# Optimization experiments

Measured on AMD Instinct MI355X. Metric: run time of the kernel, lower is better.

The kernel has to match this reference:

```python
import jax, jax.numpy as jnp
import numpy as np

D_MODEL = 1024
NHEAD = 16
HEAD_DIM = D_MODEL // NHEAD
NEG = -1e9
LN_EPS = 1e-5


def setup_inputs() -> dict:
    key = jax.random.key(0)
    ks = jax.random.split(key, 12)
    B, S, D = 2, 2048, D_MODEL
    scale = 1.0 / np.sqrt(D)
    inp = {
        "x": jax.random.normal(ks[0], (B, S, D), jnp.float32),
        "mask": jax.random.randint(ks[1], (B, S), 0, 2, jnp.int32),
        "wq": jax.random.normal(ks[2], (D, D), jnp.float32) * scale,
        "bq": jnp.zeros((D,), jnp.float32),
        "wk": jax.random.normal(ks[3], (D, D), jnp.float32) * scale,
        "bk": jnp.zeros((D,), jnp.float32),
        "wv": jax.random.normal(ks[4], (D, D), jnp.float32) * scale,
        "bv": jnp.zeros((D,), jnp.float32),
        "wo": jax.random.normal(ks[5], (D, D), jnp.float32) * scale,
        "bo": jnp.zeros((D,), jnp.float32),
        "attn_bias": jax.random.normal(ks[6], (1, NHEAD, 1, 1), jnp.float32) * 0.02,
        "ln_g": jnp.ones((D,), jnp.float32),
        "ln_b": jnp.zeros((D,), jnp.float32),
    }
    return inp


def _layer_norm(x, g, b):
    mu = jnp.mean(x, axis=-1, keepdims=True)
    var = jnp.var(x, axis=-1, keepdims=True)
    return (x - mu) * jax.lax.rsqrt(var + LN_EPS) * g + b


def reference(x, mask, wq, bq, wk, bk, wv, bv, wo, bo, attn_bias, ln_g, ln_b):
    B, S, D = x.shape
    H, Hd = NHEAD, HEAD_DIM
    # QKV projections -> [B, H, S, Hd]
    q = (x @ wq + bq).reshape(B, S, H, Hd).transpose(0, 2, 1, 3)
    k = (x @ wk + bk).reshape(B, S, H, Hd).transpose(0, 2, 1, 3)
    v = (x @ wv + bv).reshape(B, S, H, Hd).transpose(0, 2, 1, 3)
    # Scores [B, H, S, S] with per-head scalar bias
    scores = jnp.einsum("bhsd,bhtd->bhst", q, k) / jnp.sqrt(jnp.float32(Hd))
    scores = scores + attn_bias
    # mask [B,S] -> [B,1,1,S]; masked_fill where mask == 0
    m = (mask[:, None, None, :] == 0)
    scores = jnp.where(m, jnp.float32(NEG), scores)
    attn = jax.nn.softmax(scores, axis=-1)  # dropout = identity (eval)
    out = jnp.einsum("bhst,bhtd->bhsd", attn, v)
    out = out.transpose(0, 2, 1, 3).reshape(B, S, D)
    out = out @ wo + bo
    return _layer_norm(x + out, ln_g, ln_b)
```

## Files before the change

kernel.cpp:

```cpp
#include <hip/hip_runtime.h>

typedef __attribute__((ext_vector_type(8))) short short8;
typedef __attribute__((ext_vector_type(4))) float f32x4;
typedef __attribute__((ext_vector_type(16))) float f32x16;
typedef __attribute__((ext_vector_type(4))) unsigned short us4;

#define DEV __device__ __forceinline__

#define GLD16(gp, lp) __builtin_amdgcn_global_load_lds( \
    (const __attribute__((address_space(1))) void*)(gp), \
    (__attribute__((address_space(3))) void*)(lp), 16, 0, 0)

DEV unsigned short f2bf(float f) {
    union { float f; unsigned u; } v; v.f = f;
    unsigned r = v.u + 0x7fffu + ((v.u >> 16) & 1u);
    return (unsigned short)(r >> 16);
}

DEV float fexp2(float x) {
#if __has_builtin(__builtin_amdgcn_exp2f)
    return __builtin_amdgcn_exp2f(x);
#else
    return __expf(x * 0.69314718056f);
#endif
}

__global__ __launch_bounds__(256) void k_convert(const float* __restrict__ x,
                                                 unsigned short* __restrict__ xb) {
    int i = blockIdx.x * 256 + threadIdx.x;
    float4 v = ((const float4*)x)[i];
    us4 o = { f2bf(v.x), f2bf(v.y), f2bf(v.z), f2bf(v.w) };
    ((us4*)xb)[i] = o;
}

__global__ __launch_bounds__(256) void k_transw(const float* __restrict__ wq, const float* __restrict__ wk,
                                                const float* __restrict__ wv, const float* __restrict__ wo,
                                                unsigned short* __restrict__ wt) {
    __shared__ float tile[32][33];
    const int z = blockIdx.z;
    const float* src = (z == 0) ? wq : (z == 1) ? wk : (z == 2) ? wv : wo;
    unsigned short* dst = wt + (size_t)z * (1u << 20);
    const int n0 = blockIdx.x * 32, k0 = blockIdx.y * 32;
    const int tx = threadIdx.x, ty = threadIdx.y;
#pragma unroll
    for (int i = 0; i < 4; ++i)
        tile[ty + i * 8][tx] = src[(size_t)(k0 + ty + i * 8) * 1024 + n0 + tx];
    __syncthreads();
#pragma unroll
    for (int i = 0; i < 4; ++i)
        dst[(size_t)(n0 + ty + i * 8) * 1024 + k0 + tx] = f2bf(tile[tx][ty + i * 8]);
}

template <int MODE>
__global__ __launch_bounds__(256) void k_gemm(const unsigned short* __restrict__ A,
                                              const unsigned short* __restrict__ Wt,
                                              const float* __restrict__ bias,
                                              void* __restrict__ out, float scale) {
    __shared__ unsigned short lA[2][128 * 32];
    __shared__ unsigned short lB[2][64 * 32];
    const int m0 = blockIdx.y * 128, n0 = blockIdx.x * 64;
    const int tid = threadIdx.x;
    const int lane = tid & 63;
    const int w = tid >> 6, wm = w >> 1, wn = w & 1;

    const int arow0 = tid >> 2, acl = tid & 3;
    const int arow1 = (tid + 256) >> 2;
    const int brow = tid >> 2;
    const unsigned short* agp0 = A + (size_t)(m0 + arow0) * 1024 + acl * 8;
    const unsigned short* agp1 = A + (size_t)(m0 + arow1) * 1024 + acl * 8;
    const unsigned short* bgp  = Wt + (size_t)(n0 + brow) * 1024 + acl * 8;
    const int apc0 = ((arow0 << 2) | (acl ^ ((arow0 >> 1) & 3))) * 8;
    const int apc1 = ((arow1 << 2) | (acl ^ ((arow1 >> 1) & 3))) * 8;
    const int bpc  = ((brow  << 2) | (acl ^ ((brow  >> 1) & 3))) * 8;

    int ach[4], bch[2];
#pragma unroll
    for (int mt = 0; mt < 4; ++mt) {
        int row = wm * 64 + mt * 16 + (lane & 15);
        ach[mt] = ((row << 2) | ((lane >> 4) ^ ((row >> 1) & 3))) * 8;
    }
#pragma unroll
    for (int nt = 0; nt < 2; ++nt) {
        int row = wn * 32 + nt * 16 + (lane & 15);
        bch[nt] = ((row << 2) | ((lane >> 4) ^ ((row >> 1) & 3))) * 8;
    }

    f32x4 acc[4][2] = {};
    short8 ra0 = *(const short8*)agp0;
    short8 ra1 = *(const short8*)agp1;
    short8 rb0 = *(const short8*)bgp;

    for (int t = 0; t < 32; ++t) {
        unsigned short* sA = lA[t & 1];
        unsigned short* sB = lB[t & 1];
        *(short8*)(sA + apc0) = ra0;
        *(short8*)(sA + apc1) = ra1;
        *(short8*)(sB + bpc)  = rb0;
        if (t < 31) {
            ra0 = *(const short8*)(agp0 + (t + 1) * 32);
            ra1 = *(const short8*)(agp1 + (t + 1) * 32);
            rb0 = *(const short8*)(bgp  + (t + 1) * 32);
        }
        __syncthreads();
        short8 af[4], bf[2];
#pragma unroll
        for (int mt = 0; mt < 4; ++mt) af[mt] = *(const short8*)(sA + ach[mt]);
#pragma unroll
        for (int nt = 0; nt < 2; ++nt) bf[nt] = *(const short8*)(sB + bch[nt]);
#pragma unroll
        for (int mt = 0; mt < 4; ++mt)
#pragma unroll
            for (int nt = 0; nt < 2; ++nt)
                acc[mt][nt] = __builtin_amdgcn_mfma_f32_16x16x32_bf16(af[mt], bf[nt], acc[mt][nt], 0, 0, 0);
    }

#pragma unroll
    for (int nt = 0; nt < 2; ++nt) {
        const int col = n0 + wn * 32 + nt * 16 + (lane & 15);
        const float bv = bias[col];
#pragma unroll
        for (int mt = 0; mt < 4; ++mt) {
#pragma unroll
            for (int r = 0; r < 4; ++r) {
                const int row = m0 + wm * 64 + mt * 16 + (lane >> 4) * 4 + r;
                const float v = (acc[mt][nt][r] + bv) * scale;
                if (MODE == 0) {
                    int b = row >> 11, s = row & 2047, h = col >> 6, hd = col & 63;
                    ((unsigned short*)out)[(size_t)((b * 16 + h) * 2048 + s) * 64 + hd] = f2bf(v);
                } else if (MODE == 1) {
                    int b = row >> 11, s = row & 2047, h = col >> 6, hd = col & 63;
                    ((unsigned short*)out)[(size_t)((b * 16 + h) * 64 + hd) * 2048 + s] = f2bf(v);
                } else {
                    ((float*)out)[(size_t)row * 1024 + col] = v;
                }
            }
        }
    }
}

__global__ __launch_bounds__(256, 2) void k_attn(const unsigned short* __restrict__ Qb,
                                                 const unsigned short* __restrict__ Kb,
                                                 const unsigned short* __restrict__ Vt,
                                                 const int* __restrict__ mask,
                                                 const float* __restrict__ attn_bias,
                                                 unsigned short* __restrict__ ao) {
    __shared__ unsigned short ksm[2 * 4096];
    __shared__ unsigned short vsm[2 * 4096];
    __shared__ float addb[2048];
    __shared__ float lbuf[128];
    const int id = blockIdx.x;
    const int xcd = id & 7, slot = id >> 3;
    const int bh = xcd * 4 + (slot >> 4), qt = slot & 15;
    const int b = bh >> 4, h = bh & 15;
    const int tid = threadIdx.x, l = tid & 63, w = tid >> 6;
    const int q = l & 31, hi = l >> 5;

    {
        const float hb = attn_bias[h] * 1.44269504f;
        const int4* m4 = (const int4*)(mask + b * 2048);
#pragma unroll
        for (int i = 0; i < 2; ++i) {
            int idx = tid + i * 256;
            int4 m = m4[idx];
            float4 a = { m.x ? hb : -1e30f, m.y ? hb : -1e30f,
                         m.z ? hb : -1e30f, m.w ? hb : -1e30f };
            ((float4*)addb)[idx] = a;
        }
    }

    const size_t bhS = (size_t)bh * 2048;
    const unsigned short* Kbh = Kb + bhS * 64;
    const unsigned short* Vbh = Vt + (size_t)bh * 64 * 2048;
    const int q0 = qt * 128 + w * 32;

    const int srow = l >> 3;
    const int sxor = 8 * ((l & 7) ^ ((l >> 3) & 7));
    const unsigned short* Ksrc = Kbh + (size_t)(w * 16 + srow) * 64 + sxor;
    const unsigned short* Vsrc = Vbh + (size_t)(w * 16 + srow) * 2048 + sxor;
    unsigned short* lk0 = ksm + w * 1024;
    unsigned short* lv0 = vsm + w * 1024;

#define STAGE(kt_, buf_) { \
    const unsigned short* gk = Ksrc + (size_t)(kt_) * 4096; \
    const unsigned short* gv = Vsrc + (kt_) * 64; \
    unsigned short* lk = lk0 + (buf_) * 4096; \
    unsigned short* lv = lv0 + (buf_) * 4096; \
    GLD16(gk, lk); GLD16(gk + 512, lk + 512); \
    GLD16(gv, lv); GLD16(gv + 16384, lv + 512); }

    int kro[2][4], vro[2][2][2];
#pragma unroll
    for (int sub = 0; sub < 2; ++sub) {
#pragma unroll
        for (int db = 0; db < 4; ++db) {
            int key = q + sub * 32;
            kro[sub][db] = key * 128 + ((db * 32 + hi * 16) ^ ((key & 7) << 4));
        }
#pragma unroll
        for (int kg = 0; kg < 2; ++kg)
#pragma unroll
            for (int dh = 0; dh < 2; ++dh) {
                int row = q + dh * 32;
                vro[sub][kg][dh] = row * 128 + ((sub * 64 + kg * 32 + hi * 16) ^ ((row & 7) << 4));
            }
    }

    short8 qf[4];
#pragma unroll
    for (int db = 0; db < 4; ++db)
        qf[db] = *(const short8*)(Qb + (bhS + q0 + q) * 64 + db * 16 + hi * 8);

    f32x16 o0 = {}, o1 = {};
    float4 ls = { 0.f, 0.f, 0.f, 0.f };

    STAGE(0, 0);
    __syncthreads();

    for (int kt = 0; kt < 32; ++kt) {
        const int cur = kt & 1;
        if (kt < 31) STAGE(kt + 1, cur ^ 1);
        const char* kb = (const char*)(ksm + cur * 4096);
        const char* vb = (const char*)(vsm + cur * 4096);
        const float* abp = addb + kt * 64;
#pragma unroll
        for (int sub = 0; sub < 2; ++sub) {
            short8 kf0 = *(const short8*)(kb + kro[sub][0]);
            short8 kf1 = *(const short8*)(kb + kro[sub][1]);
            short8 kf2 = *(const short8*)(kb + kro[sub][2]);
            short8 kf3 = *(const short8*)(kb + kro[sub][3]);
            f32x16 sa0 = {}, sa1 = {};
            __builtin_amdgcn_s_setprio(1);
            sa0 = __builtin_amdgcn_mfma_f32_32x32x16_bf16(kf0, qf[0], sa0, 0, 0, 0);
            sa1 = __builtin_amdgcn_mfma_f32_32x32x16_bf16(kf1, qf[1], sa1, 0, 0, 0);
            sa0 = __builtin_amdgcn_mfma_f32_32x32x16_bf16(kf2, qf[2], sa0, 0, 0, 0);
            sa1 = __builtin_amdgcn_mfma_f32_32x32x16_bf16(kf3, qf[3], sa1, 0, 0, 0);
            __builtin_amdgcn_s_setprio(0);
            float p[16];
#pragma unroll
            for (int rr = 0; rr < 4; ++rr) {
                float4 ab = *(const float4*)(abp + sub * 32 + rr * 8 + hi * 4);
                p[rr * 4 + 0] = fexp2(sa0[rr * 4 + 0] + sa1[rr * 4 + 0] + ab.x);
                p[rr * 4 + 1] = fexp2(sa0[rr * 4 + 1] + sa1[rr * 4 + 1] + ab.y);
                p[rr * 4 + 2] = fexp2(sa0[rr * 4 + 2] + sa1[rr * 4 + 2] + ab.z);
                p[rr * 4 + 3] = fexp2(sa0[rr * 4 + 3] + sa1[rr * 4 + 3] + ab.w);
            }
#pragma unroll
            for (int r = 0; r < 16; r += 4) {
                ls.x += p[r]; ls.y += p[r + 1]; ls.z += p[r + 2]; ls.w += p[r + 3];
            }
#pragma unroll
            for (int kg = 0; kg < 2; ++kg) {
                unsigned P0, P1, P2, P3;
                asm("v_cvt_pk_bf16_f32 %0, %1, %2" : "=v"(P0) : "v"(p[kg * 8 + 0]), "v"(p[kg * 8 + 1]));
                asm("v_cvt_pk_bf16_f32 %0, %1, %2" : "=v"(P1) : "v"(p[kg * 8 + 2]), "v"(p[kg * 8 + 3]));
                asm("v_cvt_pk_bf16_f32 %0, %1, %2" : "=v"(P2) : "v"(p[kg * 8 + 4]), "v"(p[kg * 8 + 5]));
                asm("v_cvt_pk_bf16_f32 %0, %1, %2" : "=v"(P3) : "v"(p[kg * 8 + 6]), "v"(p[kg * 8 + 7]));
                asm("v_permlane32_swap_b32 %0, %1" : "+v"(P0), "+v"(P2));
                asm("v_permlane32_swap_b32 %0, %1" : "+v"(P1), "+v"(P3));
                union { unsigned u[4]; short8 s8; } af;
                af.u[0] = P0; af.u[1] = P1; af.u[2] = P2; af.u[3] = P3;
                short8 vf0 = *(const short8*)(vb + vro[sub][kg][0]);
                short8 vf1 = *(const short8*)(vb + vro[sub][kg][1]);
                __builtin_amdgcn_s_setprio(1);
                o0 = __builtin_amdgcn_mfma_f32_32x32x16_bf16(af.s8, vf0, o0, 0, 0, 0);
                o1 = __builtin_amdgcn_mfma_f32_32x32x16_bf16(af.s8, vf1, o1, 0, 0, 0);
                __builtin_amdgcn_s_setprio(0);
            }
        }
        __syncthreads();
    }

    float lsum = ls.x + ls.y + ls.z + ls.w;
    lsum += __shfl_xor(lsum, 32, 64);
    if (hi == 0) lbuf[w * 32 + q] = lsum;
    __syncthreads();
    float4 linv[4];
#pragma unroll
    for (int rr = 0; rr < 4; ++rr) {
        float4 lv = *(const float4*)(lbuf + w * 32 + rr * 8 + hi * 4);
        linv[rr] = { __builtin_amdgcn_rcpf(lv.x), __builtin_amdgcn_rcpf(lv.y),
                     __builtin_amdgcn_rcpf(lv.z), __builtin_amdgcn_rcpf(lv.w) };
    }
    unsigned short* aop = ao + ((size_t)b * 2048 + q0) * 1024 + h * 64 + q;
#pragma unroll
    for (int r = 0; r < 16; ++r) {
        int qrow = (r & 3) + 8 * (r >> 2) + 4 * hi;
        aop[(size_t)qrow * 1024] = f2bf(o0[r] * linv[r >> 2][r & 3]);
        aop[(size_t)qrow * 1024 + 32] = f2bf(o1[r] * linv[r >> 2][r & 3]);
    }
#undef STAGE
}

__global__ __launch_bounds__(256) void k_ln(const float* __restrict__ x, const float* __restrict__ op,
                                            const float* __restrict__ g, const float* __restrict__ be,
                                            float* __restrict__ out) {
    const int row = blockIdx.x, tid = threadIdx.x;
    const float4 xv = ((const float4*)(x + (size_t)row * 1024))[tid];
    const float4 ov = ((const float4*)(op + (size_t)row * 1024))[tid];
    float4 v = { xv.x + ov.x, xv.y + ov.y, xv.z + ov.z, xv.w + ov.w };
    float sum = v.x + v.y + v.z + v.w;
    float ss = v.x * v.x + v.y * v.y + v.z * v.z + v.w * v.w;
#pragma unroll
    for (int xm = 1; xm < 64; xm <<= 1) {
        sum += __shfl_xor(sum, xm, 64);
        ss += __shfl_xor(ss, xm, 64);
    }
    __shared__ float red[8];
    const int lane = tid & 63, w = tid >> 6;
    if (lane == 0) { red[w] = sum; red[4 + w] = ss; }
    __syncthreads();
    sum = red[0] + red[1] + red[2] + red[3];
    ss = red[4] + red[5] + red[6] + red[7];
    const float mu = sum * (1.0f / 1024.0f);
    const float rstd = rsqrtf(ss * (1.0f / 1024.0f) - mu * mu + 1e-5f);
    const float4 gv = ((const float4*)g)[tid];
    const float4 bv = ((const float4*)be)[tid];
    float4 o = { (v.x - mu) * rstd * gv.x + bv.x, (v.y - mu) * rstd * gv.y + bv.y,
                 (v.z - mu) * rstd * gv.z + bv.z, (v.w - mu) * rstd * gv.w + bv.w };
    ((float4*)(out + (size_t)row * 1024))[tid] = o;
}

extern "C" void kernel_launch(void* const* d_in, const int* in_sizes, int n_in,
                              void* d_out, int out_size, void* d_ws, size_t ws_size,
                              hipStream_t stream) {
    const float* x        = (const float*)d_in[0];
    const int*   mask     = (const int*)d_in[1];
    const float* wq       = (const float*)d_in[2];
    const float* bq       = (const float*)d_in[3];
    const float* wk       = (const float*)d_in[4];
    const float* bk       = (const float*)d_in[5];
    const float* wv       = (const float*)d_in[6];
    const float* bv       = (const float*)d_in[7];
    const float* wo       = (const float*)d_in[8];
    const float* bo       = (const float*)d_in[9];
    const float* attnb    = (const float*)d_in[10];
    const float* ln_g     = (const float*)d_in[11];
    const float* ln_b     = (const float*)d_in[12];

    char* ws = (char*)d_ws;
    unsigned short* xb  = (unsigned short*)(ws);
    unsigned short* wt  = (unsigned short*)(ws + (8ll  << 20));
    unsigned short* qb  = (unsigned short*)(ws + (16ll << 20));
    unsigned short* kb  = (unsigned short*)(ws + (24ll << 20));
    unsigned short* vtb = (unsigned short*)(ws + (32ll << 20));
    unsigned short* ao  = (unsigned short*)(ws + (40ll << 20));
    float*          opj = (float*)(ws + (48ll << 20));

    const float qscale = 0.125f * 1.44269504f;

    k_convert<<<4096, 256, 0, stream>>>(x, xb);
    k_transw<<<dim3(32, 32, 4), dim3(32, 8), 0, stream>>>(wq, wk, wv, wo, wt);
    k_gemm<0><<<dim3(16, 32), 256, 0, stream>>>(xb, wt,              bq, (void*)qb, qscale);
    k_gemm<0><<<dim3(16, 32), 256, 0, stream>>>(xb, wt + (1u << 20), bk, (void*)kb, 1.0f);
    k_gemm<1><<<dim3(16, 32), 256, 0, stream>>>(xb, wt + (2u << 20), bv, (void*)vtb, 1.0f);
    k_attn<<<512, 256, 0, stream>>>(qb, kb, vtb, mask, attnb, ao);
    k_gemm<2><<<dim3(16, 32), 256, 0, stream>>>(ao, wt + (3u << 20), bo, (void*)opj, 1.0f);
    k_ln<<<4096, 256, 0, stream>>>(x, opj, ln_g, ln_b, (float*)d_out);
}
```

Before: 148.5 us.

## Split attention over key halves, async-load GEMM tiles, bf16 output projection

Attention now splits each query tile across two key halves, giving 1024 blocks at higher occupancy. Each half writes unnormalized partial outputs and row sums, and a new combine kernel adds them and normalizes. The GEMM swaps register-staged tile loads for direct global-to-LDS loads with double buffering. The output projection is written as bf16 instead of fp32 to reduce traffic into layernorm, at the cost of an extra kernel launch, an extra round trip for the partials and lower precision in the residual add.

```diff
diff --git a/kernel.cpp b/kernel.cpp
--- a/kernel.cpp
+++ b/kernel.cpp
@@ -15,6 +15,11 @@
     union { float f; unsigned u; } v; v.f = f;
     unsigned r = v.u + 0x7fffu + ((v.u >> 16) & 1u);
     return (unsigned short)(r >> 16);
+}
+
+DEV float bf2f(unsigned short u) {
+    union { unsigned u; float f; } v; v.u = (unsigned)u << 16;
+    return v.f;
 }
 
 DEV float fexp2(float x) {
@@ -63,15 +68,18 @@
     const int lane = tid & 63;
     const int w = tid >> 6, wm = w >> 1, wn = w & 1;
 
-    const int arow0 = tid >> 2, acl = tid & 3;
-    const int arow1 = (tid + 256) >> 2;
-    const int brow = tid >> 2;
-    const unsigned short* agp0 = A + (size_t)(m0 + arow0) * 1024 + acl * 8;
-    const unsigned short* agp1 = A + (size_t)(m0 + arow1) * 1024 + acl * 8;
-    const unsigned short* bgp  = Wt + (size_t)(n0 + brow) * 1024 + acl * 8;
-    const int apc0 = ((arow0 << 2) | (acl ^ ((arow0 >> 1) & 3))) * 8;
-    const int apc1 = ((arow1 << 2) | (acl ^ ((arow1 >> 1) & 3))) * 8;
-    const int bpc  = ((brow  << 2) | (acl ^ ((brow  >> 1) & 3))) * 8;
+    const int srow = tid >> 2;
+    const int scl = (tid & 3) ^ ((tid >> 3) & 3);
+    const unsigned short* aSrc0 = A + (size_t)(m0 + srow) * 1024 + scl * 8;
+    const unsigned short* aSrc1 = A + (size_t)(m0 + 64 + srow) * 1024 + scl * 8;
+    const unsigned short* bSrc  = Wt + (size_t)(n0 + srow) * 1024 + scl * 8;
+
+#define GSTAGE(t_, buf_) { \
+    unsigned short* sA_ = lA[buf_] + w * 512; \
+    unsigned short* sB_ = lB[buf_] + w * 512; \
+    GLD16(aSrc0 + (t_) * 32, sA_); \
+    GLD16(aSrc1 + (t_) * 32, sA_ + 2048); \
+    GLD16(bSrc  + (t_) * 32, sB_); }
 
     int ach[4], bch[2];
 #pragma unroll
@@ -86,22 +94,14 @@
     }
 
     f32x4 acc[4][2] = {};
-    short8 ra0 = *(const short8*)agp0;
-    short8 ra1 = *(const short8*)agp1;
-    short8 rb0 = *(const short8*)bgp;
+    GSTAGE(0, 0);
+    __syncthreads();
 
     for (int t = 0; t < 32; ++t) {
-        unsigned short* sA = lA[t & 1];
-        unsigned short* sB = lB[t & 1];
-        *(short8*)(sA + apc0) = ra0;
-        *(short8*)(sA + apc1) = ra1;
-        *(short8*)(sB + bpc)  = rb0;
-        if (t < 31) {
-            ra0 = *(const short8*)(agp0 + (t + 1) * 32);
-            ra1 = *(const short8*)(agp1 + (t + 1) * 32);
-            rb0 = *(const short8*)(bgp  + (t + 1) * 32);
-        }
-        __syncthreads();
+        const int cur = t & 1;
+        if (t < 31) GSTAGE(t + 1, cur ^ 1);
+        const unsigned short* sA = lA[cur];
+        const unsigned short* sB = lB[cur];
         short8 af[4], bf[2];
 #pragma unroll
         for (int mt = 0; mt < 4; ++mt) af[mt] = *(const short8*)(sA + ach[mt]);
@@ -112,7 +112,9 @@
 #pragma unroll
             for (int nt = 0; nt < 2; ++nt)
                 acc[mt][nt] = __builtin_amdgcn_mfma_f32_16x16x32_bf16(af[mt], bf[nt], acc[mt][nt], 0, 0, 0);
-    }
+        __syncthreads();
+    }
+#undef GSTAGE
 
 #pragma unroll
     for (int nt = 0; nt < 2; ++nt) {
@@ -131,52 +133,49 @@
                     int b = row >> 11, s = row & 2047, h = col >> 6, hd = col & 63;
                     ((unsigned short*)out)[(size_t)((b * 16 + h) * 64 + hd) * 2048 + s] = f2bf(v);
                 } else {
-                    ((float*)out)[(size_t)row * 1024 + col] = v;
+                    ((unsigned short*)out)[(size_t)row * 1024 + col] = f2bf(v);
                 }
             }
         }
     }
 }
 
-__global__ __launch_bounds__(256, 2) void k_attn(const unsigned short* __restrict__ Qb,
+__global__ __launch_bounds__(256, 4) void k_attn(const unsigned short* __restrict__ Qb,
                                                  const unsigned short* __restrict__ Kb,
                                                  const unsigned short* __restrict__ Vt,
                                                  const int* __restrict__ mask,
                                                  const float* __restrict__ attn_bias,
-                                                 unsigned short* __restrict__ ao) {
+                                                 unsigned short* __restrict__ po0,
+                                                 unsigned short* __restrict__ po1,
+                                                 float* __restrict__ lp0,
+                                                 float* __restrict__ lp1) {
     __shared__ unsigned short ksm[2 * 4096];
     __shared__ unsigned short vsm[2 * 4096];
-    __shared__ float addb[2048];
-    __shared__ float lbuf[128];
+    __shared__ float addb[1024];
     const int id = blockIdx.x;
     const int xcd = id & 7, slot = id >> 3;
-    const int bh = xcd * 4 + (slot >> 4), qt = slot & 15;
+    const int half = slot & 1, qt = (slot >> 1) & 15, bh = xcd * 4 + (slot >> 5);
     const int b = bh >> 4, h = bh & 15;
     const int tid = threadIdx.x, l = tid & 63, w = tid >> 6;
     const int q = l & 31, hi = l >> 5;
 
     {
         const float hb = attn_bias[h] * 1.44269504f;
-        const int4* m4 = (const int4*)(mask + b * 2048);
-#pragma unroll
-        for (int i = 0; i < 2; ++i) {
-            int idx = tid + i * 256;
-            int4 m = m4[idx];
-            float4 a = { m.x ? hb : -1e30f, m.y ? hb : -1e30f,
-                         m.z ? hb : -1e30f, m.w ? hb : -1e30f };
-            ((float4*)addb)[idx] = a;
-        }
+        int4 m = ((const int4*)(mask + b * 2048 + half * 1024))[tid];
+        float4 a = { m.x ? hb : -1e30f, m.y ? hb : -1e30f,
+                     m.z ? hb : -1e30f, m.w ? hb : -1e30f };
+        ((float4*)addb)[tid] = a;
     }
 
     const size_t bhS = (size_t)bh * 2048;
-    const unsigned short* Kbh = Kb + bhS * 64;
+    const unsigned short* Kbh = Kb + (bhS + half * 1024) * 64;
     const unsigned short* Vbh = Vt + (size_t)bh * 64 * 2048;
     const int q0 = qt * 128 + w * 32;
 
     const int srow = l >> 3;
     const int sxor = 8 * ((l & 7) ^ ((l >> 3) & 7));
     const unsigned short* Ksrc = Kbh + (size_t)(w * 16 + srow) * 64 + sxor;
-    const unsigned short* Vsrc = Vbh + (size_t)(w * 16 + srow) * 2048 + sxor;
+    const unsigned short* Vsrc = Vbh + (size_t)(w * 16 + srow) * 2048 + half * 1024 + sxor;
     unsigned short* lk0 = ksm + w * 1024;
     unsigned short* lv0 = vsm + w * 1024;
 
@@ -216,9 +215,9 @@
     STAGE(0, 0);
     __syncthreads();
 
-    for (int kt = 0; kt < 32; ++kt) {
+    for (int kt = 0; kt < 16; ++kt) {
         const int cur = kt & 1;
-        if (kt < 31) STAGE(kt + 1, cur ^ 1);
+        if (kt < 15) STAGE(kt + 1, cur ^ 1);
         const char* kb = (const char*)(ksm + cur * 4096);
         const char* vb = (const char*)(vsm + cur * 4096);
         const float* abp = addb + kt * 64;
@@ -269,35 +268,48 @@
         }
         __syncthreads();
     }
+#undef STAGE
 
     float lsum = ls.x + ls.y + ls.z + ls.w;
     lsum += __shfl_xor(lsum, 32, 64);
-    if (hi == 0) lbuf[w * 32 + q] = lsum;
-    __syncthreads();
-    float4 linv[4];
-#pragma unroll
-    for (int rr = 0; rr < 4; ++rr) {
-        float4 lv = *(const float4*)(lbuf + w * 32 + rr * 8 + hi * 4);
-        linv[rr] = { __builtin_amdgcn_rcpf(lv.x), __builtin_amdgcn_rcpf(lv.y),
-                     __builtin_amdgcn_rcpf(lv.z), __builtin_amdgcn_rcpf(lv.w) };
-    }
-    unsigned short* aop = ao + ((size_t)b * 2048 + q0) * 1024 + h * 64 + q;
+    float* lpx = half ? lp1 : lp0;
+    if (hi == 0) lpx[bhS + q0 + q] = lsum;
+    unsigned short* pop = (half ? po1 : po0) + ((size_t)b * 2048 + q0) * 1024 + h * 64 + q;
 #pragma unroll
     for (int r = 0; r < 16; ++r) {
         int qrow = (r & 3) + 8 * (r >> 2) + 4 * hi;
-        aop[(size_t)qrow * 1024] = f2bf(o0[r] * linv[r >> 2][r & 3]);
-        aop[(size_t)qrow * 1024 + 32] = f2bf(o1[r] * linv[r >> 2][r & 3]);
-    }
-#undef STAGE
-}
-
-__global__ __launch_bounds__(256) void k_ln(const float* __restrict__ x, const float* __restrict__ op,
+        pop[(size_t)qrow * 1024] = f2bf(o0[r]);
+        pop[(size_t)qrow * 1024 + 32] = f2bf(o1[r]);
+    }
+}
+
+__global__ __launch_bounds__(256) void k_comb(const unsigned short* __restrict__ po0,
+                                              const unsigned short* __restrict__ po1,
+                                              const float* __restrict__ lp0,
+                                              const float* __restrict__ lp1,
+                                              unsigned short* __restrict__ ao) {
+    const int idx8 = blockIdx.x * 256 + threadIdx.x;
+    const int e = idx8 * 8;
+    const int row = e >> 10, c = e & 1023;
+    const int h = c >> 6, b = row >> 11, s = row & 2047;
+    const size_t li = ((size_t)(b * 16 + h) << 11) + s;
+    const float rinv = __builtin_amdgcn_rcpf(lp0[li] + lp1[li]);
+    short8 a0 = ((const short8*)po0)[idx8];
+    short8 a1 = ((const short8*)po1)[idx8];
+    short8 o;
+#pragma unroll
+    for (int j = 0; j < 8; ++j)
+        o[j] = (short)f2bf((bf2f((unsigned short)a0[j]) + bf2f((unsigned short)a1[j])) * rinv);
+    ((short8*)ao)[idx8] = o;
+}
+
+__global__ __launch_bounds__(256) void k_ln(const float* __restrict__ x, const unsigned short* __restrict__ op,
                                             const float* __restrict__ g, const float* __restrict__ be,
                                             float* __restrict__ out) {
     const int row = blockIdx.x, tid = threadIdx.x;
     const float4 xv = ((const float4*)(x + (size_t)row * 1024))[tid];
-    const float4 ov = ((const float4*)(op + (size_t)row * 1024))[tid];
-    float4 v = { xv.x + ov.x, xv.y + ov.y, xv.z + ov.z, xv.w + ov.w };
+    const us4 ov = ((const us4*)(op + (size_t)row * 1024))[tid];
+    float4 v = { xv.x + bf2f(ov.x), xv.y + bf2f(ov.y), xv.z + bf2f(ov.z), xv.w + bf2f(ov.w) };
     float sum = v.x + v.y + v.z + v.w;
     float ss = v.x * v.x + v.y * v.y + v.z * v.z + v.w * v.w;
 #pragma unroll
@@ -343,8 +355,12 @@
     unsigned short* qb  = (unsigned short*)(ws + (16ll << 20));
     unsigned short* kb  = (unsigned short*)(ws + (24ll << 20));
     unsigned short* vtb = (unsigned short*)(ws + (32ll << 20));
-    unsigned short* ao  = (unsigned short*)(ws + (40ll << 20));
-    float*          opj = (float*)(ws + (48ll << 20));
+    unsigned short* po1 = (unsigned short*)(ws + (40ll << 20));
+    float*          lp0 = (float*)(ws + (48ll << 20));
+    float*          lp1 = (float*)(ws + (48ll << 20) + (256ll << 10));
+    unsigned short* po0 = xb;
+    unsigned short* ao  = qb;
+    unsigned short* opj = kb;
 
     const float qscale = 0.125f * 1.44269504f;
 
@@ -353,7 +369,8 @@
     k_gemm<0><<<dim3(16, 32), 256, 0, stream>>>(xb, wt,              bq, (void*)qb, qscale);
     k_gemm<0><<<dim3(16, 32), 256, 0, stream>>>(xb, wt + (1u << 20), bk, (void*)kb, 1.0f);
     k_gemm<1><<<dim3(16, 32), 256, 0, stream>>>(xb, wt + (2u << 20), bv, (void*)vtb, 1.0f);
-    k_attn<<<512, 256, 0, stream>>>(qb, kb, vtb, mask, attnb, ao);
-    k_gemm<2><<<dim3(16, 32), 256, 0, stream>>>(ao, wt + (3u << 20), bo, (void*)opj, 1.0f);
+    k_attn<<<1024, 256, 0, stream>>>(qb, kb, vtb, mask, attnb, po0, po1, lp0, lp1);
+    k_comb<<<2048, 256, 0, stream>>>(po0, po1, lp0, lp1, ao);
+    k_gemm<3><<<dim3(16, 32), 256, 0, stream>>>(ao, wt + (3u << 20), bo, (void*)opj, 1.0f);
     k_ln<<<4096, 256, 0, stream>>>(x, opj, ln_g, ln_b, (float*)d_out);
 }
```

New measurement: 162.2 us. 1.09x slower.
